# Performance work log

Measured on AMD Instinct MI355X. Metric: run time of the kernel, lower is better.

The kernel has to match this reference:

```python
import jax, jax.numpy as jnp
import numpy as np

N, D, C = 32768, 1024, 256
GAMMA = 1e-4


def setup_inputs() -> dict:
    key = jax.random.key(0)
    kx, kw = jax.random.split(key)
    X = jax.random.normal(kx, (N, D), dtype=jnp.float32)
    # lcls linear params: weight [C, D], bias [C] (torch nn.Linear layout)
    W = jax.random.normal(kw, (C, D), dtype=jnp.float32) * (1.0 / np.sqrt(D))
    b = jnp.zeros((C,), dtype=jnp.float32)
    return {"X": X, "W": W, "b": b}


def reference(X, W, b):
    # P = softmax(X @ W.T + b) over cluster dim C
    P = jax.nn.softmax(X @ W.T + b, axis=-1)            # [N, C]
    # Reorder P @ P.T @ X -> P @ (P.T @ X): avoids the O(N^2) affinity matrix
    PtX = jnp.einsum('nc,nd->cd', P, X)                  # [C, D]
    return X + GAMMA * (P @ PtX)                         # [N, D]
```

## Files before the change

kernel.cpp:

```cpp
#include <hip/hip_runtime.h>
#include <hip/hip_bf16.h>
#include <stdint.h>

#define N_TOK 32768
#define DIM   1024
#define NC    256
#define GAMMA_F 1e-4f

typedef unsigned short u16;
typedef __attribute__((ext_vector_type(8))) short bf16x8;
typedef __attribute__((ext_vector_type(4))) float f32x4;

__device__ __forceinline__ u16 f2b(float f) {
  union { float f; uint32_t u; } c; c.f = f;
  uint32_t u = c.u;
  return (u16)((u + 0x7FFFu + ((u >> 16) & 1u)) >> 16);
}

__device__ __forceinline__ void gll16(const void* g, void* l) {
  __builtin_amdgcn_global_load_lds(
      (const __attribute__((address_space(1))) unsigned int*)g,
      (__attribute__((address_space(3))) unsigned int*)l, 16, 0, 0);
}


__global__ __launch_bounds__(256) void k0_convert_w(const float* __restrict__ W,
                                                    u16* __restrict__ Wb) {
  const int idx = (blockIdx.x * 256 + threadIdx.x) * 4;
  const float4 v = *reinterpret_cast<const float4*>(&W[idx]);
  ushort4 o;
  o.x = f2b(v.x); o.y = f2b(v.y); o.z = f2b(v.z); o.w = f2b(v.w);
  *reinterpret_cast<ushort4*>(&Wb[idx]) = o;
}

__global__ __launch_bounds__(256, 2) void p1_fused(const float* __restrict__ X,
                                                   const u16* __restrict__ Wb,
                                                   const float* __restrict__ bias,
                                                   u16* __restrict__ P,
                                                   u16* __restrict__ PT) {
  __shared__ __align__(16) char smem[40960];
  u16* As = (u16*)smem;
  u16* Bs = (u16*)(smem + 8192);
  const int t = threadIdx.x;
  const int lane = t & 63, wave = t >> 6;
  const int wm = wave & 1, wn = wave >> 1;
  const int id = blockIdx.x;
  const int n0 = ((id & 7) * 64 + (id >> 3)) * 64;
  const int frow = lane & 15, fq = lane >> 4;
  const int au = t & 7, ar0 = t >> 3;
  const int bug = (lane & 7) ^ (lane >> 3);

  f32x4 acc[2][8] = {};
  for (int kt = 0; kt < 16; ++kt) {
    const int k0 = kt * 64;
#pragma unroll
    for (int h = 0; h < 2; ++h) {
      const int r = ar0 + h * 32;
      const size_t gb = (size_t)(n0 + r) * DIM + k0 + au * 8;
      const float4 v0 = *reinterpret_cast<const float4*>(&X[gb]);
      const float4 v1 = *reinterpret_cast<const float4*>(&X[gb + 4]);
      bf16x8 u;
      u[0] = (short)f2b(v0.x); u[1] = (short)f2b(v0.y);
      u[2] = (short)f2b(v0.z); u[3] = (short)f2b(v0.w);
      u[4] = (short)f2b(v1.x); u[5] = (short)f2b(v1.y);
      u[6] = (short)f2b(v1.z); u[7] = (short)f2b(v1.w);
      *reinterpret_cast<bf16x8*>(&As[r * 64 + ((au ^ (r & 7)) * 8)]) = u;
    }
#pragma unroll
    for (int i = 0; i < 8; ++i) {
      const int chunk = wave * 8 + i;
      const int brow = chunk * 8 + (lane >> 3);
      gll16(&Wb[(size_t)brow * DIM + k0 + bug * 8], &Bs[chunk * 512]);
    }
    __syncthreads();
#pragma unroll
    for (int ks = 0; ks < 2; ++ks) {
      bf16x8 af[2], bg[8];
#pragma unroll
      for (int m = 0; m < 2; ++m) {
        const int r = wm * 32 + m * 16 + frow;
        af[m] = *reinterpret_cast<const bf16x8*>(&As[r * 64 + (((ks * 4 + fq) ^ (r & 7)) * 8)]);
      }
#pragma unroll
      for (int n = 0; n < 8; ++n) {
        const int r = wn * 128 + n * 16 + frow;
        bg[n] = *reinterpret_cast<const bf16x8*>(&Bs[r * 64 + (((ks * 4 + fq) ^ (r & 7)) * 8)]);
      }
#pragma unroll
      for (int m = 0; m < 2; ++m)
#pragma unroll
        for (int n = 0; n < 8; ++n)
          acc[m][n] = __builtin_amdgcn_mfma_f32_16x16x32_bf16(af[m], bg[n], acc[m][n], 0, 0, 0);
    }
    __syncthreads();
  }

  u16*   Su     = (u16*)smem;
  float* red_mx = (float*)(smem + 33280);
  float* red_sm = (float*)(smem + 33792);

  float bias_r[8];
#pragma unroll
  for (int n = 0; n < 8; ++n) bias_r[n] = bias[wn * 128 + n * 16 + frow];
#pragma unroll
  for (int m = 0; m < 2; ++m)
#pragma unroll
    for (int n = 0; n < 8; ++n)
#pragma unroll
      for (int j = 0; j < 4; ++j) acc[m][n][j] += bias_r[n];

  float mx[2][4];
#pragma unroll
  for (int m = 0; m < 2; ++m)
#pragma unroll
    for (int j = 0; j < 4; ++j) {
      float v = acc[m][0][j];
#pragma unroll
      for (int n = 1; n < 8; ++n) v = fmaxf(v, acc[m][n][j]);
#pragma unroll
      for (int s = 1; s < 16; s <<= 1) v = fmaxf(v, __shfl_xor(v, s, 64));
      mx[m][j] = v;
    }
  if (frow == 0) {
#pragma unroll
    for (int m = 0; m < 2; ++m)
#pragma unroll
      for (int j = 0; j < 4; ++j)
        red_mx[(wm * 32 + m * 16 + fq * 4 + j) * 2 + wn] = mx[m][j];
  }
  __syncthreads();

  const float l2e = 1.44269504088896f;
  float psum[2][4];
#pragma unroll
  for (int m = 0; m < 2; ++m)
#pragma unroll
    for (int j = 0; j < 4; ++j) {
      const int row = wm * 32 + m * 16 + fq * 4 + j;
      const float2 r2 = *reinterpret_cast<const float2*>(&red_mx[row * 2]);
      const float M = fmaxf(r2.x, r2.y);
      float s = 0.f;
#pragma unroll
      for (int n = 0; n < 8; ++n) {
        const float e = exp2f((acc[m][n][j] - M) * l2e);
        acc[m][n][j] = e;
        s += e;
      }
#pragma unroll
      for (int ss = 1; ss < 16; ss <<= 1) s += __shfl_xor(s, ss, 64);
      psum[m][j] = s;
    }
  if (frow == 0) {
#pragma unroll
    for (int m = 0; m < 2; ++m)
#pragma unroll
      for (int j = 0; j < 4; ++j)
        red_sm[(wm * 32 + m * 16 + fq * 4 + j) * 2 + wn] = psum[m][j];
  }
  __syncthreads();

#pragma unroll
  for (int m = 0; m < 2; ++m)
#pragma unroll
    for (int j = 0; j < 4; ++j) {
      const int row = wm * 32 + m * 16 + fq * 4 + j;
      const float2 r2 = *reinterpret_cast<const float2*>(&red_sm[row * 2]);
      const float iv = 1.0f / (r2.x + r2.y);
      const int sw = (row & 7) << 2;
#pragma unroll
      for (int n = 0; n < 8; ++n)
        Su[row * 260 + ((wn * 128 + n * 16 + frow) ^ sw)] = f2b(acc[m][n][j] * iv);
    }
  __syncthreads();

#pragma unroll
  for (int g = 0; g < 16; ++g) {
    const int row = g * 4 + wave;
    const int c = lane * 4;
    const ushort4 v = *reinterpret_cast<const ushort4*>(&Su[row * 260 + (c ^ ((row & 7) << 2))]);
    *reinterpret_cast<ushort4*>(&P[(size_t)(n0 + row) * NC + c]) = v;
  }
#pragma unroll
  for (int it = 0; it < 16; ++it) {
    const int c = it * 16 + wave * 4 + fq;
    const int n = frow * 4;
    ushort4 o;
    o.x = Su[(n + 0) * 260 + (c ^ (((n + 0) & 7) << 2))];
    o.y = Su[(n + 1) * 260 + (c ^ (((n + 1) & 7) << 2))];
    o.z = Su[(n + 2) * 260 + (c ^ (((n + 2) & 7) << 2))];
    o.w = Su[(n + 3) * 260 + (c ^ (((n + 3) & 7) << 2))];
    *reinterpret_cast<ushort4*>(&PT[(size_t)c * N_TOK + n0 + n]) = o;
  }
}

__global__ __launch_bounds__(256, 3) void p2_direct(const float* __restrict__ X,
                                                    const u16* __restrict__ PT,
                                                    float* __restrict__ part) {
  __shared__ __align__(16) char smem[40960];
  u16* As = (u16*)smem;
  u16* Bs = (u16*)(smem + 8192);
  const int t = threadIdx.x;
  const int lane = t & 63, wave = t >> 6;
  const int id = blockIdx.x;
  const int wgid = (id & 7) * 64 + (id >> 3);
  const int d0 = (wgid & 15) * 64;
  const int sk = wgid >> 4;
  const int frow = lane & 15, fq = lane >> 4;
  const int dloc = t & 31;
  const int kp = t >> 5;
  const int bug = (lane & 7) ^ (lane >> 3);
  f32x4 acc[4][4] = {};
  for (int kt = 0; kt < 16; ++kt) {
    const size_t nb = (size_t)sk * 1024 + kt * 64;
#pragma unroll
    for (int pass = 0; pass < 4; ++pass) {
      const int kk = pass * 16 + kp * 2;
#pragma unroll
      for (int jj = 0; jj < 2; ++jj) {
        const int d = dloc + jj * 32;
        const float x0 = X[(nb + kk) * DIM + d0 + d];
        const float x1 = X[(nb + kk + 1) * DIM + d0 + d];
        const uint32_t pk = (uint32_t)f2b(x0) | ((uint32_t)f2b(x1) << 16);
        *reinterpret_cast<uint32_t*>(&As[d * 64 + (((kk >> 3) ^ (d & 7)) * 8) + (kk & 7)]) = pk;
      }
    }
#pragma unroll
    for (int i = 0; i < 16; ++i) {
      const int ch = wave * 16 + i;
      const int c = ch * 8 + (lane >> 3);
      gll16(&PT[(size_t)c * N_TOK + nb + bug * 8], &Bs[ch * 512]);
    }
    __syncthreads();
#pragma unroll
    for (int ks = 0; ks < 2; ++ks) {
      bf16x8 af[4], bg[4];
#pragma unroll
      for (int m = 0; m < 4; ++m) {
        const int r = m * 16 + frow;
        af[m] = *reinterpret_cast<const bf16x8*>(&As[r * 64 + (((ks * 4 + fq) ^ (r & 7)) * 8)]);
      }
#pragma unroll
      for (int n = 0; n < 4; ++n) {
        const int r = wave * 64 + n * 16 + frow;
        bg[n] = *reinterpret_cast<const bf16x8*>(&Bs[r * 64 + (((ks * 4 + fq) ^ (r & 7)) * 8)]);
      }
#pragma unroll
      for (int m = 0; m < 4; ++m)
#pragma unroll
        for (int n = 0; n < 4; ++n)
          acc[m][n] = __builtin_amdgcn_mfma_f32_16x16x32_bf16(af[m], bg[n], acc[m][n], 0, 0, 0);
    }
    __syncthreads();
  }
  float* Cf = (float*)smem;
  float* pl = part + (size_t)sk * (DIM * NC);
  const int cl = (t & 63) * 4;
  const int rr = t >> 6;
#pragma unroll
  for (int h = 0; h < 2; ++h) {
    __syncthreads();
#pragma unroll
    for (int mm = 0; mm < 2; ++mm) {
      const int m = h * 2 + mm;
#pragma unroll
      for (int n = 0; n < 4; ++n) {
        const int rloc = mm * 16 + fq * 4;
        const int col = wave * 64 + n * 16 + frow;
#pragma unroll
        for (int j = 0; j < 4; ++j)
          Cf[(rloc + j) * 260 + col] = acc[m][n][j];
      }
    }
    __syncthreads();
#pragma unroll
    for (int p = 0; p < 8; ++p) {
      const int row = p * 4 + rr;
      const f32x4 v = *reinterpret_cast<const f32x4*>(&Cf[row * 260 + cl]);
      *reinterpret_cast<f32x4*>(&pl[(size_t)(d0 + h * 32 + row) * NC + cl]) = v;
    }
  }
}

__global__ __launch_bounds__(256) void k2_reduce(const float* __restrict__ part,
                                                 u16* __restrict__ PtXb) {
  const int g = (blockIdx.x * 256 + threadIdx.x) * 4;
  f32x4 s = {0.f, 0.f, 0.f, 0.f};
#pragma unroll
  for (int p = 0; p < 32; ++p)
    s += *reinterpret_cast<const f32x4*>(&part[(size_t)p * (DIM * NC) + g]);
  ushort4 o;
  o.x = f2b(s[0] * GAMMA_F); o.y = f2b(s[1] * GAMMA_F);
  o.z = f2b(s[2] * GAMMA_F); o.w = f2b(s[3] * GAMMA_F);
  *reinterpret_cast<ushort4*>(&PtXb[g]) = o;
}

__global__ __launch_bounds__(256, 3) void p3_gemm(const u16* __restrict__ P,
                                                  const u16* __restrict__ PtXb,
                                                  const float* __restrict__ X,
                                                  float* __restrict__ Out) {
  __shared__ __align__(16) char smem[34816];
  u16* As = (u16*)smem;
  u16* Bs = (u16*)(smem + 16384);
  const int t = threadIdx.x;
  const int lane = t & 63, wave = t >> 6;
  const int wm = wave & 1, wn = wave >> 1;
  const int id = blockIdx.x;
  const int swz = (id & 7) * 256 + (id >> 3);
  const int n0 = (swz & 255) * 128;
  const int d0 = (swz >> 8) * 128;
  const int frow = lane & 15, fq = lane >> 4;
  const int srow = lane >> 3;
  const int bug = (lane & 7) ^ (lane >> 3);
  f32x4 acc[4][4] = {};
  for (int kt = 0; kt < 4; ++kt) {
    const int k0 = kt * 64;
#pragma unroll
    for (int i = 0; i < 4; ++i) {
      const int chunk = wave * 4 + i;
      const int r = chunk * 8 + srow;
      gll16(&P[(size_t)(n0 + r) * NC + k0 + bug * 8], &As[chunk * 512]);
      gll16(&PtXb[(size_t)(d0 + r) * NC + k0 + bug * 8], &Bs[chunk * 512]);
    }
    __syncthreads();
#pragma unroll
    for (int ks = 0; ks < 2; ++ks) {
      bf16x8 af[4], bg[4];
#pragma unroll
      for (int m = 0; m < 4; ++m) {
        const int r = wm * 64 + m * 16 + frow;
        af[m] = *reinterpret_cast<const bf16x8*>(&As[r * 64 + (((ks * 4 + fq) ^ (r & 7)) * 8)]);
      }
#pragma unroll
      for (int n = 0; n < 4; ++n) {
        const int r = wn * 64 + n * 16 + frow;
        bg[n] = *reinterpret_cast<const bf16x8*>(&Bs[r * 64 + (((ks * 4 + fq) ^ (r & 7)) * 8)]);
      }
#pragma unroll
      for (int m = 0; m < 4; ++m)
#pragma unroll
        for (int n = 0; n < 4; ++n)
          acc[m][n] = __builtin_amdgcn_mfma_f32_16x16x32_bf16(af[m], bg[n], acc[m][n], 0, 0, 0);
    }
    __syncthreads();
  }
  float* Cf = (float*)smem;
  const int cl = (t & 31) * 4;
  const int rq = t >> 5;
#pragma unroll
  for (int h = 0; h < 2; ++h) {
    __syncthreads();
    if (wm == h) {
#pragma unroll
      for (int m = 0; m < 4; ++m)
#pragma unroll
        for (int n = 0; n < 4; ++n) {
          const int rr = m * 16 + fq * 4;
          const int col = wn * 64 + n * 16 + frow;
#pragma unroll
          for (int j = 0; j < 4; ++j)
            Cf[(rr + j) * 132 + col] = acc[m][n][j];
        }
    }
    __syncthreads();
#pragma unroll
    for (int p = 0; p < 8; ++p) {
      const int row = p * 8 + rq;
      float4 v = *reinterpret_cast<const float4*>(&Cf[row * 132 + cl]);
      const size_t off = (size_t)(n0 + h * 64 + row) * DIM + d0 + cl;
      const float4 x = *reinterpret_cast<const float4*>(&X[off]);
      v.x += x.x; v.y += x.y; v.z += x.z; v.w += x.w;
      *reinterpret_cast<float4*>(&Out[off]) = v;
    }
  }
}

extern "C" void kernel_launch(void* const* d_in, const int* in_sizes, int n_in,
                              void* d_out, int out_size, void* d_ws, size_t ws_size,
                              hipStream_t stream) {
  const float* X = (const float*)d_in[0];
  const float* W = (const float*)d_in[1];
  const float* b = (const float*)d_in[2];
  float* Out = (float*)d_out;
  char* ws = (char*)d_ws;

  const size_t OFF_WB   = 0;
  const size_t OFF_PTXB = (size_t)512 << 10;
  const size_t OFF_PART = (size_t)1 << 20;
  const size_t OFF_P    = (size_t)34 << 20;
  const size_t OFF_PT   = (size_t)50 << 20;
  const size_t NEED     = (size_t)66 << 20;
  if (ws_size < NEED) return;

  u16*   Wb   = (u16*)(ws + OFF_WB);
  u16*   PtXb = (u16*)(ws + OFF_PTXB);
  float* part = (float*)(ws + OFF_PART);
  u16*   Pp   = (u16*)(ws + OFF_P);
  u16*   PT   = (u16*)(ws + OFF_PT);

  k0_convert_w<<<dim3((NC * DIM) / 1024), 256, 0, stream>>>(W, Wb);
  p1_fused<<<dim3(N_TOK / 64), 256, 0, stream>>>(X, Wb, b, Pp, PT);
  p2_direct<<<dim3(512), 256, 0, stream>>>(X, PT, part);
  k2_reduce<<<dim3((DIM * NC) / 1024), 256, 0, stream>>>(part, PtXb);
  p3_gemm<<<dim3(2048), 256, 0, stream>>>(Pp, PtXb, X, Out);
}
```

Baseline: 354.0 us.

## Halve p1 row tile to 32 and double p2 split-K count

p1_fused now handles 32 tokens per block instead of 64. Each wave owns a 64-column slice of all 256 clusters, and the softmax reduction is redone across 4 waves. The block count doubles and the launch bound allows 4 blocks per CU. p2_direct is split into 64 K-partitions of 512 tokens, giving 1024 blocks, so k2_reduce now sums 64 partials and the workspace grows. The goal is more parallelism and occupancy across the CUs. The cost is twice as many W tile reloads in p1 and twice the partial-sum traffic in the reduction.

```diff
diff --git a/kernel.cpp b/kernel.cpp
--- a/kernel.cpp
+++ b/kernel.cpp
@@ -33,30 +33,27 @@
   *reinterpret_cast<ushort4*>(&Wb[idx]) = o;
 }
 
-__global__ __launch_bounds__(256, 2) void p1_fused(const float* __restrict__ X,
+__global__ __launch_bounds__(256, 4) void p1_fused(const float* __restrict__ X,
                                                    const u16* __restrict__ Wb,
                                                    const float* __restrict__ bias,
                                                    u16* __restrict__ P,
                                                    u16* __restrict__ PT) {
-  __shared__ __align__(16) char smem[40960];
+  __shared__ __align__(16) char smem[36864];
   u16* As = (u16*)smem;
-  u16* Bs = (u16*)(smem + 8192);
+  u16* Bs = (u16*)(smem + 4096);
   const int t = threadIdx.x;
   const int lane = t & 63, wave = t >> 6;
-  const int wm = wave & 1, wn = wave >> 1;
   const int id = blockIdx.x;
-  const int n0 = ((id & 7) * 64 + (id >> 3)) * 64;
+  const int n0 = ((id & 7) * 128 + (id >> 3)) * 32;
   const int frow = lane & 15, fq = lane >> 4;
-  const int au = t & 7, ar0 = t >> 3;
+  const int au = t & 7, ar = t >> 3;
   const int bug = (lane & 7) ^ (lane >> 3);
 
-  f32x4 acc[2][8] = {};
+  f32x4 acc[2][4] = {};
   for (int kt = 0; kt < 16; ++kt) {
     const int k0 = kt * 64;
-#pragma unroll
-    for (int h = 0; h < 2; ++h) {
-      const int r = ar0 + h * 32;
-      const size_t gb = (size_t)(n0 + r) * DIM + k0 + au * 8;
+    {
+      const size_t gb = (size_t)(n0 + ar) * DIM + k0 + au * 8;
       const float4 v0 = *reinterpret_cast<const float4*>(&X[gb]);
       const float4 v1 = *reinterpret_cast<const float4*>(&X[gb + 4]);
       bf16x8 u;
@@ -64,7 +61,7 @@
       u[2] = (short)f2b(v0.z); u[3] = (short)f2b(v0.w);
       u[4] = (short)f2b(v1.x); u[5] = (short)f2b(v1.y);
       u[6] = (short)f2b(v1.z); u[7] = (short)f2b(v1.w);
-      *reinterpret_cast<bf16x8*>(&As[r * 64 + ((au ^ (r & 7)) * 8)]) = u;
+      *reinterpret_cast<bf16x8*>(&As[ar * 64 + ((au ^ (ar & 7)) * 8)]) = u;
     }
 #pragma unroll
     for (int i = 0; i < 8; ++i) {
@@ -75,121 +72,105 @@
     __syncthreads();
 #pragma unroll
     for (int ks = 0; ks < 2; ++ks) {
-      bf16x8 af[2], bg[8];
+      bf16x8 af[2], bg[4];
 #pragma unroll
       for (int m = 0; m < 2; ++m) {
-        const int r = wm * 32 + m * 16 + frow;
+        const int r = m * 16 + frow;
         af[m] = *reinterpret_cast<const bf16x8*>(&As[r * 64 + (((ks * 4 + fq) ^ (r & 7)) * 8)]);
       }
 #pragma unroll
-      for (int n = 0; n < 8; ++n) {
-        const int r = wn * 128 + n * 16 + frow;
+      for (int n = 0; n < 4; ++n) {
+        const int r = wave * 64 + n * 16 + frow;
         bg[n] = *reinterpret_cast<const bf16x8*>(&Bs[r * 64 + (((ks * 4 + fq) ^ (r & 7)) * 8)]);
       }
 #pragma unroll
       for (int m = 0; m < 2; ++m)
 #pragma unroll
-        for (int n = 0; n < 8; ++n)
+        for (int n = 0; n < 4; ++n)
           acc[m][n] = __builtin_amdgcn_mfma_f32_16x16x32_bf16(af[m], bg[n], acc[m][n], 0, 0, 0);
     }
     __syncthreads();
   }
 
   u16*   Su     = (u16*)smem;
-  float* red_mx = (float*)(smem + 33280);
-  float* red_sm = (float*)(smem + 33792);
-
-  float bias_r[8];
-#pragma unroll
-  for (int n = 0; n < 8; ++n) bias_r[n] = bias[wn * 128 + n * 16 + frow];
+  float* red_mx = (float*)(smem + 16640);
+  float* red_sm = (float*)(smem + 17152);
+
+  float bias_r[4];
+#pragma unroll
+  for (int n = 0; n < 4; ++n) bias_r[n] = bias[wave * 64 + n * 16 + frow];
 #pragma unroll
   for (int m = 0; m < 2; ++m)
 #pragma unroll
-    for (int n = 0; n < 8; ++n)
+    for (int n = 0; n < 4; ++n)
 #pragma unroll
       for (int j = 0; j < 4; ++j) acc[m][n][j] += bias_r[n];
 
-  float mx[2][4];
 #pragma unroll
   for (int m = 0; m < 2; ++m)
 #pragma unroll
     for (int j = 0; j < 4; ++j) {
       float v = acc[m][0][j];
 #pragma unroll
-      for (int n = 1; n < 8; ++n) v = fmaxf(v, acc[m][n][j]);
+      for (int n = 1; n < 4; ++n) v = fmaxf(v, acc[m][n][j]);
 #pragma unroll
       for (int s = 1; s < 16; s <<= 1) v = fmaxf(v, __shfl_xor(v, s, 64));
-      mx[m][j] = v;
-    }
-  if (frow == 0) {
-#pragma unroll
-    for (int m = 0; m < 2; ++m)
-#pragma unroll
-      for (int j = 0; j < 4; ++j)
-        red_mx[(wm * 32 + m * 16 + fq * 4 + j) * 2 + wn] = mx[m][j];
-  }
+      if (frow == 0) red_mx[(m * 16 + fq * 4 + j) * 4 + wave] = v;
+    }
   __syncthreads();
 
   const float l2e = 1.44269504088896f;
-  float psum[2][4];
 #pragma unroll
   for (int m = 0; m < 2; ++m)
 #pragma unroll
     for (int j = 0; j < 4; ++j) {
-      const int row = wm * 32 + m * 16 + fq * 4 + j;
-      const float2 r2 = *reinterpret_cast<const float2*>(&red_mx[row * 2]);
-      const float M = fmaxf(r2.x, r2.y);
+      const int row = m * 16 + fq * 4 + j;
+      const f32x4 r4 = *reinterpret_cast<const f32x4*>(&red_mx[row * 4]);
+      const float M = fmaxf(fmaxf(r4[0], r4[1]), fmaxf(r4[2], r4[3]));
       float s = 0.f;
 #pragma unroll
-      for (int n = 0; n < 8; ++n) {
+      for (int n = 0; n < 4; ++n) {
         const float e = exp2f((acc[m][n][j] - M) * l2e);
         acc[m][n][j] = e;
         s += e;
       }
 #pragma unroll
       for (int ss = 1; ss < 16; ss <<= 1) s += __shfl_xor(s, ss, 64);
-      psum[m][j] = s;
-    }
-  if (frow == 0) {
-#pragma unroll
-    for (int m = 0; m < 2; ++m)
-#pragma unroll
-      for (int j = 0; j < 4; ++j)
-        red_sm[(wm * 32 + m * 16 + fq * 4 + j) * 2 + wn] = psum[m][j];
-  }
+      if (frow == 0) red_sm[row * 4 + wave] = s;
+    }
   __syncthreads();
 
 #pragma unroll
   for (int m = 0; m < 2; ++m)
 #pragma unroll
     for (int j = 0; j < 4; ++j) {
-      const int row = wm * 32 + m * 16 + fq * 4 + j;
-      const float2 r2 = *reinterpret_cast<const float2*>(&red_sm[row * 2]);
-      const float iv = 1.0f / (r2.x + r2.y);
+      const int row = m * 16 + fq * 4 + j;
+      const f32x4 r4 = *reinterpret_cast<const f32x4*>(&red_sm[row * 4]);
+      const float iv = 1.0f / (r4[0] + r4[1] + r4[2] + r4[3]);
       const int sw = (row & 7) << 2;
 #pragma unroll
-      for (int n = 0; n < 8; ++n)
-        Su[row * 260 + ((wn * 128 + n * 16 + frow) ^ sw)] = f2b(acc[m][n][j] * iv);
+      for (int n = 0; n < 4; ++n)
+        Su[row * 260 + ((wave * 64 + n * 16 + frow) ^ sw)] = f2b(acc[m][n][j] * iv);
     }
   __syncthreads();
 
 #pragma unroll
-  for (int g = 0; g < 16; ++g) {
+  for (int g = 0; g < 8; ++g) {
     const int row = g * 4 + wave;
     const int c = lane * 4;
     const ushort4 v = *reinterpret_cast<const ushort4*>(&Su[row * 260 + (c ^ ((row & 7) << 2))]);
     *reinterpret_cast<ushort4*>(&P[(size_t)(n0 + row) * NC + c]) = v;
   }
 #pragma unroll
-  for (int it = 0; it < 16; ++it) {
-    const int c = it * 16 + wave * 4 + fq;
-    const int n = frow * 4;
+  for (int it = 0; it < 8; ++it) {
+    const int c = it * 32 + (t >> 3);
+    const int nn = (t & 7) * 4;
     ushort4 o;
-    o.x = Su[(n + 0) * 260 + (c ^ (((n + 0) & 7) << 2))];
-    o.y = Su[(n + 1) * 260 + (c ^ (((n + 1) & 7) << 2))];
-    o.z = Su[(n + 2) * 260 + (c ^ (((n + 2) & 7) << 2))];
-    o.w = Su[(n + 3) * 260 + (c ^ (((n + 3) & 7) << 2))];
-    *reinterpret_cast<ushort4*>(&PT[(size_t)c * N_TOK + n0 + n]) = o;
+    o.x = Su[(nn + 0) * 260 + (c ^ (((nn + 0) & 7) << 2))];
+    o.y = Su[(nn + 1) * 260 + (c ^ (((nn + 1) & 7) << 2))];
+    o.z = Su[(nn + 2) * 260 + (c ^ (((nn + 2) & 7) << 2))];
+    o.w = Su[(nn + 3) * 260 + (c ^ (((nn + 3) & 7) << 2))];
+    *reinterpret_cast<ushort4*>(&PT[(size_t)c * N_TOK + n0 + nn]) = o;
   }
 }
 
@@ -202,7 +183,7 @@
   const int t = threadIdx.x;
   const int lane = t & 63, wave = t >> 6;
   const int id = blockIdx.x;
-  const int wgid = (id & 7) * 64 + (id >> 3);
+  const int wgid = (id & 7) * 128 + (id >> 3);
   const int d0 = (wgid & 15) * 64;
   const int sk = wgid >> 4;
   const int frow = lane & 15, fq = lane >> 4;
@@ -210,8 +191,8 @@
   const int kp = t >> 5;
   const int bug = (lane & 7) ^ (lane >> 3);
   f32x4 acc[4][4] = {};
-  for (int kt = 0; kt < 16; ++kt) {
-    const size_t nb = (size_t)sk * 1024 + kt * 64;
+  for (int kt = 0; kt < 8; ++kt) {
+    const size_t nb = (size_t)sk * 512 + kt * 64;
 #pragma unroll
     for (int pass = 0; pass < 4; ++pass) {
       const int kk = pass * 16 + kp * 2;
@@ -225,8 +206,8 @@
       }
     }
 #pragma unroll
-    for (int i = 0; i < 16; ++i) {
-      const int ch = wave * 16 + i;
+    for (int i = 0; i < 8; ++i) {
+      const int ch = wave * 8 + i;
       const int c = ch * 8 + (lane >> 3);
       gll16(&PT[(size_t)c * N_TOK + nb + bug * 8], &Bs[ch * 512]);
     }
@@ -286,7 +267,7 @@
   const int g = (blockIdx.x * 256 + threadIdx.x) * 4;
   f32x4 s = {0.f, 0.f, 0.f, 0.f};
 #pragma unroll
-  for (int p = 0; p < 32; ++p)
+  for (int p = 0; p < 64; ++p)
     s += *reinterpret_cast<const f32x4*>(&part[(size_t)p * (DIM * NC) + g]);
   ushort4 o;
   o.x = f2b(s[0] * GAMMA_F); o.y = f2b(s[1] * GAMMA_F);
@@ -386,9 +367,9 @@
   const size_t OFF_WB   = 0;
   const size_t OFF_PTXB = (size_t)512 << 10;
   const size_t OFF_PART = (size_t)1 << 20;
-  const size_t OFF_P    = (size_t)34 << 20;
-  const size_t OFF_PT   = (size_t)50 << 20;
-  const size_t NEED     = (size_t)66 << 20;
+  const size_t OFF_P    = (size_t)66 << 20;
+  const size_t OFF_PT   = (size_t)82 << 20;
+  const size_t NEED     = (size_t)98 << 20;
   if (ws_size < NEED) return;
 
   u16*   Wb   = (u16*)(ws + OFF_WB);
@@ -398,8 +379,8 @@
   u16*   PT   = (u16*)(ws + OFF_PT);
 
   k0_convert_w<<<dim3((NC * DIM) / 1024), 256, 0, stream>>>(W, Wb);
-  p1_fused<<<dim3(N_TOK / 64), 256, 0, stream>>>(X, Wb, b, Pp, PT);
-  p2_direct<<<dim3(512), 256, 0, stream>>>(X, PT, part);
+  p1_fused<<<dim3(N_TOK / 32), 256, 0, stream>>>(X, Wb, b, Pp, PT);
+  p2_direct<<<dim3(1024), 256, 0, stream>>>(X, PT, part);
   k2_reduce<<<dim3((DIM * NC) / 1024), 256, 0, stream>>>(part, PtXb);
   p3_gemm<<<dim3(2048), 256, 0, stream>>>(Pp, PtXb, X, Out);
 }
```

Measured after the change: 364.9 us. +3.1%, slower.
